# Performance work log

Hardware: AMD Instinct MI355X
Metric: run time of the kernel (lower is better)

Reference implementation:

```python
import jax, jax.numpy as jnp
import numpy as np

E = 1024
H = 8
D = E // H
WINDOW = 256
EPS = 1e-5


def layernorm(x, w, b):
    mu = jnp.mean(x, axis=-1, keepdims=True)
    var = jnp.mean((x - mu) ** 2, axis=-1, keepdims=True)
    return (x - mu) * jax.lax.rsqrt(var + EPS) * w + b


def setup_inputs() -> dict:
    key = jax.random.key(0)
    ks = jax.random.split(key, 12)
    B, T = 2, 2048
    s = 1.0 / np.sqrt(E)
    return {
        "x": jax.random.normal(ks[0], (B, T, E), jnp.float32),
        "ln1_w": jnp.ones((E,), jnp.float32),
        "ln1_b": jnp.zeros((E,), jnp.float32),
        "ln2_w": jnp.ones((E,), jnp.float32),
        "ln2_b": jnp.zeros((E,), jnp.float32),
        "in_proj_w": jax.random.normal(ks[1], (3 * E, E), jnp.float32) * s,
        "in_proj_b": jnp.zeros((3 * E,), jnp.float32),
        "out_w": jax.random.normal(ks[2], (E, E), jnp.float32) * s,
        "out_b": jnp.zeros((E,), jnp.float32),
        "w1": jax.random.normal(ks[3], (4 * E, E), jnp.float32) * s,
        "b1": jnp.zeros((4 * E,), jnp.float32),
        "w2": jax.random.normal(ks[4], (E, 4 * E), jnp.float32) * (1.0 / np.sqrt(4 * E)),
        "b2": jnp.zeros((E,), jnp.float32),
    }


def reference(x, ln1_w, ln1_b, ln2_w, ln2_b, in_proj_w, in_proj_b, out_w, out_b, w1, b1, w2, b2):
    B, T, _ = x.shape
    h = layernorm(x, ln1_w, ln1_b)
    # qkv projection: torch Linear is x @ W.T + b
    qkv = h @ in_proj_w.T + in_proj_b  # [B,T,3E]
    q, k, v = jnp.split(qkv, 3, axis=-1)
    q = q.reshape(B, T, H, D).transpose(0, 2, 1, 3)  # [B,H,T,D]
    k = k.reshape(B, T, H, D).transpose(0, 2, 1, 3)
    v = v.reshape(B, T, H, D).transpose(0, 2, 1, 3)
    scores = jnp.einsum("bhqd,bhkd->bhqk", q, k) / np.sqrt(D)
    idx = jnp.arange(T)
    row = idx[:, None]
    col = idx[None, :]
    # masked where future (col>row) OR outside window (col < row - WINDOW)
    allowed = (col <= row) & (col >= row - WINDOW)
    scores = jnp.where(allowed, scores, -jnp.inf)
    attn = jax.nn.softmax(scores, axis=-1)
    out = jnp.einsum("bhqk,bhkd->bhqd", attn, v)  # [B,H,T,D]
    out = out.transpose(0, 2, 1, 3).reshape(B, T, E)
    out = out @ out_w.T + out_b
    h2 = x + out
    m = layernorm(h2, ln2_w, ln2_b)
    m = jax.nn.relu(m @ w1.T + b1) @ w2.T + b2
    return h2 + m
```

## Files before the change

kernel.cpp:

```cpp
#include <hip/hip_runtime.h>

#define TOK 4096
#define EMB 1024

typedef __attribute__((ext_vector_type(8))) short s16x8;
typedef __attribute__((ext_vector_type(4))) float f32x4;

__device__ __forceinline__ unsigned short f2bf(float f) {
  union { float f; unsigned int u; } v; v.f = f;
  unsigned int r = v.u + 0x7FFFu + ((v.u >> 16) & 1u);
  return (unsigned short)(r >> 16);
}
__device__ __forceinline__ float bf2f(unsigned short u) {
  union { unsigned int u; float f; } v; v.u = ((unsigned int)u) << 16; return v.f;
}

#define GLOAD_LDS16(g, l) __builtin_amdgcn_global_load_lds( \
    (const __attribute__((address_space(1))) void*)(g), \
    (__attribute__((address_space(3))) void*)(l), 16, 0, 0)

template<int RELU>
__global__ __launch_bounds__(512)
void gemm256(const unsigned short* __restrict__ A,
             const unsigned short* __restrict__ B,
             const float* __restrict__ bias,
             unsigned short* __restrict__ C, int M, int N, int K)
{
  __shared__ unsigned short lds[2][2][256 * 64];
  const int tid = threadIdx.x;
  const int lane = tid & 63;
  const int w = tid >> 6;
  const int wr = w >> 2, wc = w & 3;
  const int l15 = lane & 15, lhi = lane >> 4;
  const int nbm = M >> 8;
  const int bm = blockIdx.x % nbm, bn = blockIdx.x / nbm;
  const int m0 = bm << 8, n0 = bn << 8;
  const int NT = K >> 6;

  const char* Abase = (const char*)(A + (size_t)m0 * K);
  const char* Bbase = (const char*)(B + (size_t)n0 * K);
  const size_t rowb = (size_t)K * 2;

  const int srt = tid >> 3;
  const int sccx = ((tid & 7) << 4) ^ ((srt & 7) << 4);

  auto stage = [&](const char* Gb, int kt, int h, int ab, int buf) {
    char* ldsb = (char*)&lds[buf][ab][0] + h * 16384 + (w << 10);
    const char* g = Gb + (size_t)(h * 128 + srt) * rowb + kt * 128 + sccx;
    GLOAD_LDS16(g, ldsb);
    GLOAD_LDS16(g + 64 * rowb, ldsb + 8192);
  };

  const int rdxor = (l15 & 7) << 4;
  auto rdA = [&](int buf, int mf, int ks) -> s16x8 {
    const int r = wr * 128 + mf * 16 + l15;
    const int cc = (ks * 64 + lhi * 16) ^ rdxor;
    return *(const s16x8*)((const char*)&lds[buf][0][0] + r * 128 + cc);
  };
  auto rdB = [&](int buf, int nf, int ks) -> s16x8 {
    const int r = wc * 64 + nf * 16 + l15;
    const int cc = (ks * 64 + lhi * 16) ^ rdxor;
    return *(const s16x8*)((const char*)&lds[buf][1][0] + r * 128 + cc);
  };

  f32x4 acc[8][4];
#pragma unroll
  for (int mf = 0; mf < 8; ++mf)
#pragma unroll
    for (int nf = 0; nf < 4; ++nf)
#pragma unroll
      for (int j = 0; j < 4; ++j) acc[mf][nf][j] = 0.f;

  stage(Abase, 0, 0, 0, 0); stage(Abase, 0, 1, 0, 0);
  stage(Bbase, 0, 0, 1, 0); stage(Bbase, 0, 1, 1, 0);
  stage(Abase, 1, 0, 0, 1); stage(Abase, 1, 1, 0, 1);
  stage(Bbase, 1, 0, 1, 1);
  asm volatile("s_waitcnt vmcnt(6)" ::: "memory");
  __builtin_amdgcn_s_barrier();

  s16x8 af[4][2], af2[4][2], bf0[2][2], bf1[2][2];

  for (int kt = 0; kt < NT; ++kt) {
    const int p = kt & 1;

#pragma unroll
    for (int mi = 0; mi < 4; ++mi) { af[mi][0] = rdA(p, mi, 0); af[mi][1] = rdA(p, mi, 1); }
#pragma unroll
    for (int ni = 0; ni < 2; ++ni) { bf0[ni][0] = rdB(p, ni, 0); bf0[ni][1] = rdB(p, ni, 1); }
    if (kt + 1 < NT) stage(Bbase, kt + 1, 1, 1, p ^ 1);
    __builtin_amdgcn_s_barrier();
    asm volatile("s_waitcnt lgkmcnt(0)" ::: "memory");
    __builtin_amdgcn_sched_barrier(0);
    __builtin_amdgcn_s_setprio(1);
#pragma unroll
    for (int mi = 0; mi < 4; ++mi)
#pragma unroll
      for (int ni = 0; ni < 2; ++ni)
#pragma unroll
        for (int ks = 0; ks < 2; ++ks)
          acc[mi][ni] = __builtin_amdgcn_mfma_f32_16x16x32_bf16(af[mi][ks], bf0[ni][ks], acc[mi][ni], 0, 0, 0);
    __builtin_amdgcn_s_setprio(0);
    __builtin_amdgcn_s_barrier();

#pragma unroll
    for (int mi = 0; mi < 4; ++mi) { af2[mi][0] = rdA(p, 4 + mi, 0); af2[mi][1] = rdA(p, 4 + mi, 1); }
#pragma unroll
    for (int ni = 0; ni < 2; ++ni) { bf1[ni][0] = rdB(p, 2 + ni, 0); bf1[ni][1] = rdB(p, 2 + ni, 1); }
    __builtin_amdgcn_s_barrier();
    asm volatile("s_waitcnt lgkmcnt(0)" ::: "memory");
    __builtin_amdgcn_sched_barrier(0);
    __builtin_amdgcn_s_setprio(1);
#pragma unroll
    for (int mi = 0; mi < 4; ++mi)
#pragma unroll
      for (int ni = 0; ni < 2; ++ni)
#pragma unroll
        for (int ks = 0; ks < 2; ++ks)
          acc[4 + mi][ni] = __builtin_amdgcn_mfma_f32_16x16x32_bf16(af2[mi][ks], bf0[ni][ks], acc[4 + mi][ni], 0, 0, 0);
    __builtin_amdgcn_s_setprio(0);
    __builtin_amdgcn_s_barrier();

    if (kt + 2 < NT) { stage(Abase, kt + 2, 0, 0, p); stage(Bbase, kt + 2, 0, 1, p); }
    __builtin_amdgcn_s_barrier();
    __builtin_amdgcn_s_setprio(1);
#pragma unroll
    for (int mi = 0; mi < 4; ++mi)
#pragma unroll
      for (int ni = 0; ni < 2; ++ni)
#pragma unroll
        for (int ks = 0; ks < 2; ++ks)
          acc[mi][2 + ni] = __builtin_amdgcn_mfma_f32_16x16x32_bf16(af[mi][ks], bf1[ni][ks], acc[mi][2 + ni], 0, 0, 0);
    __builtin_amdgcn_s_setprio(0);
    __builtin_amdgcn_s_barrier();

    if (kt + 2 < NT) stage(Abase, kt + 2, 1, 0, p);
    __builtin_amdgcn_s_barrier();
    __builtin_amdgcn_s_setprio(1);
#pragma unroll
    for (int mi = 0; mi < 4; ++mi)
#pragma unroll
      for (int ni = 0; ni < 2; ++ni)
#pragma unroll
        for (int ks = 0; ks < 2; ++ks)
          acc[4 + mi][2 + ni] = __builtin_amdgcn_mfma_f32_16x16x32_bf16(af2[mi][ks], bf1[ni][ks], acc[4 + mi][2 + ni], 0, 0, 0);
    __builtin_amdgcn_s_setprio(0);
    if (kt + 1 < NT) {
      if (kt + 2 < NT) asm volatile("s_waitcnt vmcnt(6)" ::: "memory");
      else             asm volatile("s_waitcnt vmcnt(0)" ::: "memory");
      __builtin_amdgcn_s_barrier();
    }
  }

#pragma unroll
  for (int mf = 0; mf < 8; ++mf) {
    const int row = m0 + wr * 128 + mf * 16 + lhi * 4;
#pragma unroll
    for (int nf = 0; nf < 4; ++nf) {
      const int col = n0 + wc * 64 + nf * 16 + l15;
      const float bv = bias[col];
#pragma unroll
      for (int j = 0; j < 4; ++j) {
        float v = acc[mf][nf][j] + bv;
        if (RELU) v = fmaxf(v, 0.f);
        C[(size_t)(row + j) * N + col] = f2bf(v);
      }
    }
  }
}

__global__ __launch_bounds__(256)
void gemm_bt_sk(const unsigned short* __restrict__ A,
                const unsigned short* __restrict__ B,
                unsigned short* __restrict__ Cpart, int M, int N, int K, int Kc)
{
  __shared__ unsigned short As[128 * 64];
  __shared__ unsigned short Bs[128 * 64];
  const int tid = threadIdx.x;
  const int lane = tid & 63;
  const int w = tid >> 6;
  const int wr = w >> 1, wc = w & 1;
  const int l15 = lane & 15, lhi = lane >> 4;
  const int nbm = M >> 7;
  const int bm = blockIdx.x % nbm;
  const int bn = blockIdx.x / nbm;
  const int m0 = bm << 7, n0 = bn << 7;
  const int k0 = blockIdx.y * Kc;

  f32x4 acc[4][4];
#pragma unroll
  for (int m = 0; m < 4; ++m)
#pragma unroll
    for (int n = 0; n < 4; ++n)
#pragma unroll
      for (int j = 0; j < 4; ++j) acc[m][n][j] = 0.f;

  const int trow = tid >> 3, tcol = (tid & 7) << 3;
  const unsigned short* Ag = A + (size_t)(m0 + trow) * K + tcol;
  const unsigned short* Bg = B + (size_t)(n0 + trow) * K + tcol;
  unsigned short* Adst = As + (w << 9);
  unsigned short* Bdst = Bs + (w << 9);

  for (int kt = k0; kt < k0 + Kc; kt += 64) {
    __syncthreads();
#pragma unroll
    for (int i = 0; i < 4; ++i) {
      GLOAD_LDS16(Ag + (size_t)(i * 32) * K + kt, Adst + i * 2048);
      GLOAD_LDS16(Bg + (size_t)(i * 32) * K + kt, Bdst + i * 2048);
    }
    __syncthreads();
#pragma unroll
    for (int ks = 0; ks < 2; ++ks) {
      s16x8 af[4], bfr[4];
#pragma unroll
      for (int m = 0; m < 4; ++m)
        af[m] = *(const s16x8*)(As + ((wr * 64 + m * 16 + l15) << 6) + ks * 32 + lhi * 8);
#pragma unroll
      for (int n = 0; n < 4; ++n)
        bfr[n] = *(const s16x8*)(Bs + ((wc * 64 + n * 16 + l15) << 6) + ks * 32 + lhi * 8);
#pragma unroll
      for (int m = 0; m < 4; ++m)
#pragma unroll
        for (int n = 0; n < 4; ++n)
          acc[m][n] = __builtin_amdgcn_mfma_f32_16x16x32_bf16(af[m], bfr[n], acc[m][n], 0, 0, 0);
    }
  }

  unsigned short* Cp = Cpart + (size_t)blockIdx.y * M * N;
#pragma unroll
  for (int m = 0; m < 4; ++m) {
    const int row = m0 + wr * 64 + m * 16 + lhi * 4;
#pragma unroll
    for (int n = 0; n < 4; ++n) {
      const int col = n0 + wc * 64 + n * 16 + l15;
#pragma unroll
      for (int j = 0; j < 4; ++j)
        Cp[(size_t)(row + j) * N + col] = f2bf(acc[m][n][j]);
    }
  }
}

__global__ __launch_bounds__(256)
void reduce_add(const unsigned short* __restrict__ part, const float* __restrict__ res,
                const float* __restrict__ bias, float* __restrict__ out,
                int MN, int N, int S)
{
  const int i4 = (blockIdx.x * 256 + threadIdx.x) * 4;
  if (i4 >= MN) return;
  const int col = i4 & (N - 1);
  float4 v = *(const float4*)(res + i4);
  v.x += bias[col]; v.y += bias[col + 1]; v.z += bias[col + 2]; v.w += bias[col + 3];
  for (int s = 0; s < S; ++s) {
    const ushort4 p = *(const ushort4*)(part + (size_t)s * MN + i4);
    v.x += bf2f(p.x); v.y += bf2f(p.y); v.z += bf2f(p.z); v.w += bf2f(p.w);
  }
  *(float4*)(out + i4) = v;
}

__global__ __launch_bounds__(256)
void reduce_ln(const unsigned short* __restrict__ part, const float* __restrict__ x,
               const float* __restrict__ ob, const float* __restrict__ ln_w,
               const float* __restrict__ ln_b, float* __restrict__ h2,
               unsigned short* __restrict__ m_in, int S)
{
  const int row = blockIdx.x;
  const int t = threadIdx.x;
  const size_t off = (size_t)row * EMB + t * 4;
  float4 v = *(const float4*)(x + off);
  const float4 obv = ((const float4*)ob)[t];
  v.x += obv.x; v.y += obv.y; v.z += obv.z; v.w += obv.w;
  for (int s = 0; s < S; ++s) {
    const ushort4 p = *(const ushort4*)(part + (size_t)s * TOK * EMB + off);
    v.x += bf2f(p.x); v.y += bf2f(p.y); v.z += bf2f(p.z); v.w += bf2f(p.w);
  }
  *(float4*)(h2 + off) = v;

  float s1 = v.x + v.y + v.z + v.w;
  float s2 = v.x * v.x + v.y * v.y + v.z * v.z + v.w * v.w;
#pragma unroll
  for (int o = 1; o < 64; o <<= 1) { s1 += __shfl_xor(s1, o); s2 += __shfl_xor(s2, o); }
  __shared__ float red[8];
  if ((t & 63) == 0) { red[t >> 6] = s1; red[4 + (t >> 6)] = s2; }
  __syncthreads();
  s1 = red[0] + red[1] + red[2] + red[3];
  s2 = red[4] + red[5] + red[6] + red[7];
  const float mu = s1 * (1.f / EMB);
  const float rs = rsqrtf(s2 * (1.f / EMB) - mu * mu + 1e-5f);
  const float4 wv = ((const float4*)ln_w)[t];
  const float4 bv = ((const float4*)ln_b)[t];
  ushort4 o;
  o.x = f2bf((v.x - mu) * rs * wv.x + bv.x);
  o.y = f2bf((v.y - mu) * rs * wv.y + bv.y);
  o.z = f2bf((v.z - mu) * rs * wv.z + bv.z);
  o.w = f2bf((v.w - mu) * rs * wv.w + bv.w);
  ((ushort4*)(m_in + (size_t)row * EMB))[t] = o;
}

__global__ __launch_bounds__(256)
void ln_bf16(const float* __restrict__ x, const float* __restrict__ wt,
             const float* __restrict__ bs, unsigned short* __restrict__ out)
{
  const int row = blockIdx.x;
  const int t = threadIdx.x;
  const float4 v = ((const float4*)(x + (size_t)row * EMB))[t];
  float s = v.x + v.y + v.z + v.w;
  float s2 = v.x * v.x + v.y * v.y + v.z * v.z + v.w * v.w;
#pragma unroll
  for (int off = 1; off < 64; off <<= 1) { s += __shfl_xor(s, off); s2 += __shfl_xor(s2, off); }
  __shared__ float red[8];
  if ((t & 63) == 0) { red[t >> 6] = s; red[4 + (t >> 6)] = s2; }
  __syncthreads();
  s = red[0] + red[1] + red[2] + red[3];
  s2 = red[4] + red[5] + red[6] + red[7];
  const float mu = s * (1.f / EMB);
  const float rs = rsqrtf(s2 * (1.f / EMB) - mu * mu + 1e-5f);
  const float4 wv = ((const float4*)wt)[t];
  const float4 bv = ((const float4*)bs)[t];
  ushort4 o;
  o.x = f2bf((v.x - mu) * rs * wv.x + bv.x);
  o.y = f2bf((v.y - mu) * rs * wv.y + bv.y);
  o.z = f2bf((v.z - mu) * rs * wv.z + bv.z);
  o.w = f2bf((v.w - mu) * rs * wv.w + bv.w);
  ((ushort4*)(out + (size_t)row * EMB))[t] = o;
}

#define Q0 786432
#define Q1 (Q0 + 262144)
#define Q2 (Q1 + 1048576)
#define Q3 (Q2 + 1048576)
__global__ __launch_bounds__(256)
void cvt4(const float* __restrict__ s0, const float* __restrict__ s1,
          const float* __restrict__ s2, const float* __restrict__ s3,
          unsigned short* __restrict__ d0, unsigned short* __restrict__ d1,
          unsigned short* __restrict__ d2, unsigned short* __restrict__ d3)
{
  const int i = blockIdx.x * 256 + threadIdx.x;
  const float* s; unsigned short* d; int off;
  if (i < Q0)      { s = s0; d = d0; off = i; }
  else if (i < Q1) { s = s1; d = d1; off = i - Q0; }
  else if (i < Q2) { s = s2; d = d2; off = i - Q1; }
  else             { s = s3; d = d3; off = i - Q2; }
  const float4 v = ((const float4*)s)[off];
  ushort4 o;
  o.x = f2bf(v.x); o.y = f2bf(v.y); o.z = f2bf(v.z); o.w = f2bf(v.w);
  ((ushort4*)d)[off] = o;
}

__global__ __launch_bounds__(256)
void attn_win(const unsigned short* __restrict__ qkv, unsigned short* __restrict__ aout)
{
  __shared__ unsigned short Ks[64 * 136];
  __shared__ unsigned short Vt[128 * 72];
  __shared__ unsigned short Ps[4 * 16 * 72];
  const int bh = blockIdx.y;
  const int b = bh >> 3, hh = bh & 7;
  const int q0 = blockIdx.x << 6;
  const int tid = threadIdx.x, lane = tid & 63, w = tid >> 6;
  const int l15 = lane & 15, lhi = lane >> 4;
  const size_t base = (size_t)b * 2048 * 3072;

  s16x8 qf[4];
  {
    const unsigned short* qp = qkv + base + (size_t)(q0 + w * 16 + l15) * 3072 + hh * 128 + lhi * 8;
#pragma unroll
    for (int ks = 0; ks < 4; ++ks) qf[ks] = *(const s16x8*)(qp + ks * 32);
  }

  f32x4 o[8];
#pragma unroll
  for (int n = 0; n < 8; ++n)
#pragma unroll
    for (int j = 0; j < 4; ++j) o[n][j] = 0.f;
  float mrow[4] = {-1e30f, -1e30f, -1e30f, -1e30f};
  float lrow[4] = {0.f, 0.f, 0.f, 0.f};

  for (int t = 0; t < 5; ++t) {
    const int kt0 = q0 - 256 + t * 64;
    if (kt0 < 0) continue;
    __syncthreads();
    {
      const unsigned short* kg = qkv + base + (size_t)kt0 * 3072 + 1024 + hh * 128;
#pragma unroll
      for (int i = 0; i < 4; ++i) {
        const int c = tid + i * 256;
        const int r = c >> 4, cc = (c & 15) << 3;
        *(s16x8*)(Ks + r * 136 + cc) = *(const s16x8*)(kg + (size_t)r * 3072 + cc);
      }
      const unsigned short* vg = qkv + base + (size_t)kt0 * 3072 + 2048 + hh * 128;
#pragma unroll
      for (int i = 0; i < 2; ++i) {
        const int c = tid + i * 256;
        const int r2 = c >> 4, cc = (c & 15) << 3;
        s16x8 v0 = *(const s16x8*)(vg + (size_t)(2 * r2) * 3072 + cc);
        s16x8 v1 = *(const s16x8*)(vg + (size_t)(2 * r2 + 1) * 3072 + cc);
#pragma unroll
        for (int jj = 0; jj < 8; ++jj) {
          unsigned int pk = (unsigned int)(unsigned short)v0[jj] |
                            ((unsigned int)(unsigned short)v1[jj] << 16);
          *(unsigned int*)(Vt + (cc + jj) * 72 + 2 * r2) = pk;
        }
      }
    }
    __syncthreads();

    f32x4 s[4];
#pragma unroll
    for (int n = 0; n < 4; ++n)
#pragma unroll
      for (int j = 0; j < 4; ++j) s[n][j] = 0.f;
#pragma unroll
    for (int ks = 0; ks < 4; ++ks) {
#pragma unroll
      for (int n = 0; n < 4; ++n) {
        s16x8 kf = *(const s16x8*)(Ks + (n * 16 + l15) * 136 + ks * 32 + lhi * 8);
        s[n] = __builtin_amdgcn_mfma_f32_16x16x32_bf16(qf[ks], kf, s[n], 0, 0, 0);
      }
    }
    const bool mlo = (t == 0);
    const bool mhi = (kt0 == q0);
#pragma unroll
    for (int n = 0; n < 4; ++n) {
      const int kcol = n * 16 + l15;
#pragma unroll
      for (int j = 0; j < 4; ++j) {
        const int qrow = w * 16 + lhi * 4 + j;
        float v = s[n][j] * 0.08838834764831845f;
        if ((mlo && kcol < qrow) || (mhi && kcol > qrow)) v = -1e30f;
        s[n][j] = v;
      }
    }
    float alpha[4];
#pragma unroll
    for (int j = 0; j < 4; ++j) {
      float mx = fmaxf(fmaxf(s[0][j], s[1][j]), fmaxf(s[2][j], s[3][j]));
#pragma unroll
      for (int off = 1; off < 16; off <<= 1) mx = fmaxf(mx, __shfl_xor(mx, off));
      const float mn = fmaxf(mrow[j], mx);
      alpha[j] = __expf(mrow[j] - mn);
      mrow[j] = mn;
    }
    float rowsum[4] = {0.f, 0.f, 0.f, 0.f};
#pragma unroll
    for (int n = 0; n < 4; ++n)
#pragma unroll
      for (int j = 0; j < 4; ++j) {
        const float p = __expf(s[n][j] - mrow[j]);
        rowsum[j] += p;
        Ps[(w * 16 + lhi * 4 + j) * 72 + n * 16 + l15] = f2bf(p);
      }
#pragma unroll
    for (int j = 0; j < 4; ++j) {
      float rs = rowsum[j];
#pragma unroll
      for (int off = 1; off < 16; off <<= 1) rs += __shfl_xor(rs, off);
      lrow[j] = lrow[j] * alpha[j] + rs;
    }
#pragma unroll
    for (int n = 0; n < 8; ++n)
#pragma unroll
      for (int j = 0; j < 4; ++j) o[n][j] *= alpha[j];
#pragma unroll
    for (int ks = 0; ks < 2; ++ks) {
      const s16x8 pf = *(const s16x8*)(Ps + (w * 16 + l15) * 72 + ks * 32 + lhi * 8);
#pragma unroll
      for (int n = 0; n < 8; ++n) {
        const s16x8 vf = *(const s16x8*)(Vt + (n * 16 + l15) * 72 + ks * 32 + lhi * 8);
        o[n] = __builtin_amdgcn_mfma_f32_16x16x32_bf16(pf, vf, o[n], 0, 0, 0);
      }
    }
  }
  unsigned short* op = aout + (size_t)(b * 2048 + q0 + w * 16) * 1024 + hh * 128;
#pragma unroll
  for (int n = 0; n < 8; ++n)
#pragma unroll
    for (int j = 0; j < 4; ++j)
      op[(size_t)(lhi * 4 + j) * 1024 + n * 16 + l15] = f2bf(o[n][j] / lrow[j]);
}

extern "C" void kernel_launch(void* const* d_in, const int* in_sizes, int n_in,
                              void* d_out, int out_size, void* d_ws, size_t ws_size,
                              hipStream_t stream)
{
  (void)in_sizes; (void)n_in; (void)out_size; (void)ws_size;
  const float* x         = (const float*)d_in[0];
  const float* ln1_w     = (const float*)d_in[1];
  const float* ln1_b     = (const float*)d_in[2];
  const float* ln2_w     = (const float*)d_in[3];
  const float* ln2_b     = (const float*)d_in[4];
  const float* in_proj_w = (const float*)d_in[5];
  const float* in_proj_b = (const float*)d_in[6];
  const float* out_w     = (const float*)d_in[7];
  const float* out_b     = (const float*)d_in[8];
  const float* w1        = (const float*)d_in[9];
  const float* b1        = (const float*)d_in[10];
  const float* w2        = (const float*)d_in[11];
  const float* b2        = (const float*)d_in[12];
  float* out = (float*)d_out;

  char* ws = (char*)d_ws;
  unsigned short* h    = (unsigned short*)(ws);
  unsigned short* wqkv = (unsigned short*)(ws + (8u << 20));
  unsigned short* wout = (unsigned short*)(ws + (14u << 20));
  unsigned short* w1b  = (unsigned short*)(ws + (16u << 20));
  unsigned short* w2b  = (unsigned short*)(ws + (24u << 20));
  unsigned short* qkv  = (unsigned short*)(ws + (32u << 20));
  unsigned short* aout = (unsigned short*)(ws + (56u << 20));
  float*          h2   = (float*)(ws + (64u << 20));
  unsigned short* m_in = (unsigned short*)(ws + (80u << 20));
  unsigned short* act  = (unsigned short*)(ws + (88u << 20));
  unsigned short* part_op = (unsigned short*)(ws + (88u << 20));
  unsigned short* part_m2 = (unsigned short*)(ws + (32u << 20));

  cvt4<<<dim3(Q3 / 256), 256, 0, stream>>>(in_proj_w, out_w, w1, w2, wqkv, wout, w1b, w2b);
  ln_bf16<<<dim3(TOK), 256, 0, stream>>>(x, ln1_w, ln1_b, h);

  gemm256<0><<<dim3(16 * 12), 512, 0, stream>>>(h, wqkv, in_proj_b, qkv, 4096, 3072, 1024);
  attn_win<<<dim3(32, 16), 256, 0, stream>>>(qkv, aout);

  gemm_bt_sk<<<dim3(32 * 8, 2), 256, 0, stream>>>(aout, wout, part_op, 4096, 1024, 1024, 512);
  reduce_ln<<<dim3(TOK), 256, 0, stream>>>(part_op, x, out_b, ln2_w, ln2_b, h2, m_in, 2);

  gemm256<1><<<dim3(16 * 16), 512, 0, stream>>>(m_in, w1b, b1, act, 4096, 4096, 1024);

  gemm_bt_sk<<<dim3(32 * 8, 4), 256, 0, stream>>>(act, w2b, part_m2, 4096, 1024, 4096, 1024);
  reduce_add<<<dim3(4096 * 1024 / 4 / 256), 256, 0, stream>>>(part_m2, h2, b2, out, 4096 * 1024, 1024, 4);
}
```

Baseline: 210.7 us.

## Run split-K GEMMs through the pipelined 256x256 kernel and drop gemm_bt_sk

Adds a split-K mode to the double-buffered 256x256 gemm256 kernel: a K offset comes from blockIdx.y, and the output goes to per-split bf16 partials with no bias. The simpler single-buffered 128x128 gemm_bt_sk is removed. The out-projection and FFN-down GEMMs now use the pipelined kernel with 4 K-splits, aiming for more data reuse per tile and overlap of loads with MFMA. In exchange, the out-projection now writes 4 partials instead of 2, so reduce_ln reads more data, and each out-projection block runs a very short K loop of only 4 tiles.

```diff
diff --git a/kernel.cpp b/kernel.cpp
--- a/kernel.cpp
+++ b/kernel.cpp
@@ -19,12 +19,12 @@
     (const __attribute__((address_space(1))) void*)(g), \
     (__attribute__((address_space(3))) void*)(l), 16, 0, 0)
 
-template<int RELU>
+template<int RELU, int PART>
 __global__ __launch_bounds__(512)
 void gemm256(const unsigned short* __restrict__ A,
              const unsigned short* __restrict__ B,
              const float* __restrict__ bias,
-             unsigned short* __restrict__ C, int M, int N, int K)
+             unsigned short* __restrict__ C, int M, int N, int K, int Kc)
 {
   __shared__ unsigned short lds[2][2][256 * 64];
   const int tid = threadIdx.x;
@@ -35,10 +35,11 @@
   const int nbm = M >> 8;
   const int bm = blockIdx.x % nbm, bn = blockIdx.x / nbm;
   const int m0 = bm << 8, n0 = bn << 8;
-  const int NT = K >> 6;
-
-  const char* Abase = (const char*)(A + (size_t)m0 * K);
-  const char* Bbase = (const char*)(B + (size_t)n0 * K);
+  const int k0 = blockIdx.y * Kc;
+  const int NT = Kc >> 6;
+
+  const char* Abase = (const char*)(A + (size_t)m0 * K) + (size_t)k0 * 2;
+  const char* Bbase = (const char*)(B + (size_t)n0 * K) + (size_t)k0 * 2;
   const size_t rowb = (size_t)K * 2;
 
   const int srt = tid >> 3;
@@ -151,90 +152,20 @@
     }
   }
 
+  unsigned short* Cw = PART ? C + (size_t)blockIdx.y * M * N : C;
 #pragma unroll
   for (int mf = 0; mf < 8; ++mf) {
     const int row = m0 + wr * 128 + mf * 16 + lhi * 4;
 #pragma unroll
     for (int nf = 0; nf < 4; ++nf) {
       const int col = n0 + wc * 64 + nf * 16 + l15;
-      const float bv = bias[col];
+      const float bv = PART ? 0.f : bias[col];
 #pragma unroll
       for (int j = 0; j < 4; ++j) {
         float v = acc[mf][nf][j] + bv;
         if (RELU) v = fmaxf(v, 0.f);
-        C[(size_t)(row + j) * N + col] = f2bf(v);
-      }
-    }
-  }
-}
-
-__global__ __launch_bounds__(256)
-void gemm_bt_sk(const unsigned short* __restrict__ A,
-                const unsigned short* __restrict__ B,
-                unsigned short* __restrict__ Cpart, int M, int N, int K, int Kc)
-{
-  __shared__ unsigned short As[128 * 64];
-  __shared__ unsigned short Bs[128 * 64];
-  const int tid = threadIdx.x;
-  const int lane = tid & 63;
-  const int w = tid >> 6;
-  const int wr = w >> 1, wc = w & 1;
-  const int l15 = lane & 15, lhi = lane >> 4;
-  const int nbm = M >> 7;
-  const int bm = blockIdx.x % nbm;
-  const int bn = blockIdx.x / nbm;
-  const int m0 = bm << 7, n0 = bn << 7;
-  const int k0 = blockIdx.y * Kc;
-
-  f32x4 acc[4][4];
-#pragma unroll
-  for (int m = 0; m < 4; ++m)
-#pragma unroll
-    for (int n = 0; n < 4; ++n)
-#pragma unroll
-      for (int j = 0; j < 4; ++j) acc[m][n][j] = 0.f;
-
-  const int trow = tid >> 3, tcol = (tid & 7) << 3;
-  const unsigned short* Ag = A + (size_t)(m0 + trow) * K + tcol;
-  const unsigned short* Bg = B + (size_t)(n0 + trow) * K + tcol;
-  unsigned short* Adst = As + (w << 9);
-  unsigned short* Bdst = Bs + (w << 9);
-
-  for (int kt = k0; kt < k0 + Kc; kt += 64) {
-    __syncthreads();
-#pragma unroll
-    for (int i = 0; i < 4; ++i) {
-      GLOAD_LDS16(Ag + (size_t)(i * 32) * K + kt, Adst + i * 2048);
-      GLOAD_LDS16(Bg + (size_t)(i * 32) * K + kt, Bdst + i * 2048);
-    }
-    __syncthreads();
-#pragma unroll
-    for (int ks = 0; ks < 2; ++ks) {
-      s16x8 af[4], bfr[4];
-#pragma unroll
-      for (int m = 0; m < 4; ++m)
-        af[m] = *(const s16x8*)(As + ((wr * 64 + m * 16 + l15) << 6) + ks * 32 + lhi * 8);
-#pragma unroll
-      for (int n = 0; n < 4; ++n)
-        bfr[n] = *(const s16x8*)(Bs + ((wc * 64 + n * 16 + l15) << 6) + ks * 32 + lhi * 8);
-#pragma unroll
-      for (int m = 0; m < 4; ++m)
-#pragma unroll
-        for (int n = 0; n < 4; ++n)
-          acc[m][n] = __builtin_amdgcn_mfma_f32_16x16x32_bf16(af[m], bfr[n], acc[m][n], 0, 0, 0);
-    }
-  }
-
-  unsigned short* Cp = Cpart + (size_t)blockIdx.y * M * N;
-#pragma unroll
-  for (int m = 0; m < 4; ++m) {
-    const int row = m0 + wr * 64 + m * 16 + lhi * 4;
-#pragma unroll
-    for (int n = 0; n < 4; ++n) {
-      const int col = n0 + wc * 64 + n * 16 + l15;
-#pragma unroll
-      for (int j = 0; j < 4; ++j)
-        Cp[(size_t)(row + j) * N + col] = f2bf(acc[m][n][j]);
+        Cw[(size_t)(row + j) * N + col] = f2bf(v);
+      }
     }
   }
 }
@@ -513,14 +444,14 @@
   cvt4<<<dim3(Q3 / 256), 256, 0, stream>>>(in_proj_w, out_w, w1, w2, wqkv, wout, w1b, w2b);
   ln_bf16<<<dim3(TOK), 256, 0, stream>>>(x, ln1_w, ln1_b, h);
 
-  gemm256<0><<<dim3(16 * 12), 512, 0, stream>>>(h, wqkv, in_proj_b, qkv, 4096, 3072, 1024);
+  gemm256<0, 0><<<dim3(16 * 12), 512, 0, stream>>>(h, wqkv, in_proj_b, qkv, 4096, 3072, 1024, 1024);
   attn_win<<<dim3(32, 16), 256, 0, stream>>>(qkv, aout);
 
-  gemm_bt_sk<<<dim3(32 * 8, 2), 256, 0, stream>>>(aout, wout, part_op, 4096, 1024, 1024, 512);
-  reduce_ln<<<dim3(TOK), 256, 0, stream>>>(part_op, x, out_b, ln2_w, ln2_b, h2, m_in, 2);
-
-  gemm256<1><<<dim3(16 * 16), 512, 0, stream>>>(m_in, w1b, b1, act, 4096, 4096, 1024);
-
-  gemm_bt_sk<<<dim3(32 * 8, 4), 256, 0, stream>>>(act, w2b, part_m2, 4096, 1024, 4096, 1024);
+  gemm256<0, 1><<<dim3(16 * 4, 4), 512, 0, stream>>>(aout, wout, nullptr, part_op, 4096, 1024, 1024, 256);
+  reduce_ln<<<dim3(TOK), 256, 0, stream>>>(part_op, x, out_b, ln2_w, ln2_b, h2, m_in, 4);
+
+  gemm256<1, 0><<<dim3(16 * 16), 512, 0, stream>>>(m_in, w1b, b1, act, 4096, 4096, 1024, 1024);
+
+  gemm256<0, 1><<<dim3(16 * 4, 4), 512, 0, stream>>>(act, w2b, nullptr, part_m2, 4096, 1024, 4096, 1024);
   reduce_add<<<dim3(4096 * 1024 / 4 / 256), 256, 0, stream>>>(part_m2, h2, b2, out, 4096 * 1024, 1024, 4);
 }
```

Result: faster. 199.6 us (-5.3%).
